# Performance work log

Hardware: AMD Instinct MI355X
Metric: run time of the kernel (lower is better)

Reference implementation:

```python
import math
import jax, jax.numpy as jnp
import numpy as np

SR = 48000
FRAME_HOP = 240
F0_MIN = 20.0
F0_MAX = 5000.0
F0_BINS = 64
VEL_DIM = 8
N_HARM = 128
NOISE_FFT = 1024
N_NOISE = NOISE_FFT // 2 + 1
HOP = NOISE_FFT // 4
PAD = NOISE_FFT // 2


def lin_interp(x, size):
    # matches F.interpolate(mode='linear', align_corners=False) along last axis
    T_in = x.shape[-1]
    pos = (jnp.arange(size, dtype=jnp.float32) + 0.5) * (T_in / size) - 0.5
    pos = jnp.clip(pos, 0.0, T_in - 1.0)
    lo = jnp.floor(pos).astype(jnp.int32)
    hi = jnp.minimum(lo + 1, T_in - 1)
    fr = pos - lo.astype(jnp.float32)
    return x[..., lo] * (1.0 - fr) + x[..., hi] * fr


def encode_f0(f0):
    f0s = jnp.clip(f0, F0_MIN, None)
    fn = jnp.clip((jnp.log(f0s) - math.log(F0_MIN)) / (math.log(F0_MAX) - math.log(F0_MIN)), 0.0, 1.0)
    i = jnp.arange(1, F0_BINS // 2 + 1, dtype=jnp.float32)
    ang = math.pi * i * fn[..., None]  # (B,T,bins/2)
    enc = jnp.stack([jnp.sin(ang), jnp.cos(ang)], axis=-1).reshape(f0.shape + (F0_BINS,))
    return enc * (f0 > 0).astype(jnp.float32)[..., None]


def encode_velocity(vel):
    vn = jnp.clip(vel.astype(jnp.float32) / 7.0, 0.0, 1.0)
    i = jnp.arange(1, VEL_DIM // 2 + 1, dtype=jnp.float32)
    ang = math.pi * i * vn[..., None]
    return jnp.stack([jnp.sin(ang), jnp.cos(ang)], axis=-1).reshape(vel.shape + (VEL_DIM,))


def gru(x, W_ih, W_hh, b_ih, b_hh):
    # torch nn.GRU, 1 layer, batch_first; gate order r,z,n
    B, T, _ = x.shape
    H = W_hh.shape[1]
    gi = x @ W_ih.T + b_ih  # (B,T,3H)

    def step(h, g):
        gh = h @ W_hh.T + b_hh
        ir, iz, in_ = jnp.split(g, 3, axis=-1)
        hr, hz, hn = jnp.split(gh, 3, axis=-1)
        r = jax.nn.sigmoid(ir + hr)
        z = jax.nn.sigmoid(iz + hz)
        n = jnp.tanh(in_ + r * hn)
        h = (1.0 - z) * n + z * h
        return h, h

    _, hs = jax.lax.scan(step, jnp.zeros((B, H), x.dtype), jnp.swapaxes(gi, 0, 1))
    return jnp.swapaxes(hs, 0, 1)


def harmonic_synth(harm_amps, f0_hz, n_samples, inh):
    # harm_amps (B,T,N), f0_hz (B,T), inh (B,) -> (B,S)
    B, T, N = harm_amps.shape
    a = lin_interp(jnp.transpose(harm_amps, (0, 2, 1)), n_samples)        # (B,N,S)
    f0_up = lin_interp(f0_hz[:, None, :], n_samples)[:, 0]               # (B,S)
    k = jnp.arange(1, N + 1, dtype=jnp.float32)
    stretch = jnp.sqrt(1.0 + inh[:, None] * k ** 2)                      # (B,N)
    inst_freq = f0_up[:, None, :] * (k[None, :] * stretch)[:, :, None]   # (B,N,S)
    mask = (inst_freq < SR * 0.45).astype(a.dtype)
    f0_mean = f0_up.mean(axis=-1)
    n_active = jnp.maximum((k[None, :] * f0_mean[:, None] < SR * 0.45).sum(axis=1), 1).astype(a.dtype)
    phase = jnp.cumsum(2.0 * jnp.pi * inst_freq / SR, axis=-1)
    sig = (a * mask * jnp.sin(phase)).sum(axis=1)
    return sig / n_active[:, None]


def noise_synth(noise_mags, f0_hz, n_samples, noise):
    # noise_mags (B,T,513), noise (B,S) -> (B,S)
    B, T, N = noise_mags.shape
    window = 0.5 - 0.5 * jnp.cos(2.0 * jnp.pi * jnp.arange(NOISE_FFT, dtype=jnp.float32) / NOISE_FFT)  # hann, periodic
    padded = jnp.pad(noise, ((0, 0), (PAD, PAD)), mode='reflect')
    T_stft = 1 + n_samples // HOP
    idx = jnp.arange(T_stft)[:, None] * HOP + jnp.arange(NOISE_FFT)[None, :]  # (T_stft, n_fft)
    frames = padded[:, idx] * window                                          # (B,T_stft,n_fft)
    spec = jnp.fft.rfft(frames)                                               # (B,T_stft,513)
    mag_up = lin_interp(jnp.transpose(noise_mags, (0, 2, 1)), T_stft)         # (B,513,T_stft)
    f0_mean = jnp.clip(f0_hz, F0_MIN, None).mean(axis=1)                      # (B,)
    freqs = jnp.arange(N_NOISE, dtype=jnp.float32) * (SR / NOISE_FFT)
    src = jnp.clip(freqs[None, :] / f0_mean[:, None] * (N / N_HARM), 0.0, N - 1.0)  # (B,513)
    lo = src.astype(jnp.int32)
    hi = jnp.minimum(lo + 1, N - 1)
    fr = (src - lo.astype(jnp.float32))[:, :, None]
    lo_e = jnp.broadcast_to(lo[:, :, None], (B, N_NOISE, T_stft))
    hi_e = jnp.broadcast_to(hi[:, :, None], (B, N_NOISE, T_stft))
    v_lo = jnp.take_along_axis(mag_up, lo_e, axis=1)
    v_hi = jnp.take_along_axis(mag_up, hi_e, axis=1)
    mag_abs = v_lo + fr * (v_hi - v_lo)                                       # (B,513,T_stft)
    shaped = spec * jnp.transpose(mag_abs, (0, 2, 1))                         # (B,T_stft,513)
    tframes = jnp.fft.irfft(shaped, n=NOISE_FFT) * window                     # (B,T_stft,n_fft)
    Lp = NOISE_FFT + (T_stft - 1) * HOP
    flat = idx.reshape(-1)
    ola = jnp.zeros((B, Lp), jnp.float32).at[:, flat].add(tframes.reshape(B, -1))
    wsq = jnp.zeros((Lp,), jnp.float32).at[flat].add(jnp.tile(window ** 2, T_stft))
    out = ola / jnp.where(wsq > 1e-11, wsq, 1.0)
    return out[:, PAD:PAD + n_samples]


def ddsp_forward(f0_hz, loudness_db, noise_L, noise_R,
                 W_pre1, b_pre1, W_pre2, b_pre2, W_ih, W_hh, b_ih, b_hh,
                 W_post, b_post, W_harm, b_harm, W_amp, b_amp,
                 W_noise, b_noise, W_namp, b_namp, W_B, b_B, velocity):
    B, T = f0_hz.shape
    n_samples = T * FRAME_HOP
    feat = jnp.concatenate([encode_f0(f0_hz),
                            jnp.broadcast_to(encode_velocity(velocity)[:, None, :], (B, T, VEL_DIM))], axis=-1)
    feat = jax.nn.relu(feat @ W_pre1 + b_pre1)
    feat = jax.nn.relu(feat @ W_pre2 + b_pre2)
    feat = gru(feat, W_ih, W_hh, b_ih, b_hh)
    feat = jax.nn.relu(feat @ W_post + b_post)
    # stereo heads stacked on channel axis c in {L,R}
    harm_dist = jax.nn.softmax(jnp.einsum('btd,cdn->cbtn', feat, W_harm) + b_harm[:, None, None, :], axis=-1)
    harm_amp = jax.nn.softplus(jnp.einsum('btd,cd->cbt', feat, W_amp) + b_amp[:, None, None])
    harm_amps = harm_dist * harm_amp[..., None]                               # (2,B,T,128)
    nmag = jax.nn.sigmoid(jnp.einsum('btd,cdn->cbtn', feat, W_noise) + b_noise[:, None, None, :])
    nmag = nmag * jax.nn.softplus(jnp.einsum('btd,cd->cbt', feat, W_namp) + b_namp[:, None, None])[..., None]
    f0_mean = jnp.clip(f0_hz, F0_MIN, None).mean(axis=1)
    midi = 69.0 + 12.0 * jnp.log2(f0_mean / 440.0)
    b_max = 0.0008 * jnp.exp(-(midi - 21.0) / 88.0 * math.log(10.0))
    inh = jax.nn.sigmoid(feat @ W_B + b_B[0]).mean(axis=1) * b_max           # inh_scale = 1.0
    hL = harmonic_synth(harm_amps[0], f0_hz, n_samples, inh)
    hR = harmonic_synth(harm_amps[1], f0_hz, n_samples, inh)
    nL = noise_synth(nmag[0], f0_hz, n_samples, noise_L)
    nR = noise_synth(nmag[1], f0_hz, n_samples, noise_R)
    lo_up = lin_interp((10.0 ** (loudness_db / 20.0))[:, None, :], n_samples)[:, 0]
    return jnp.stack([(hL + nL) * lo_up, (hR + nR) * lo_up], axis=1)         # (B,2,S)


def setup_inputs() -> dict:
    key = jax.random.key(0)
    ks = iter(jax.random.split(key, 40))
    B, T = 2, 400
    S = T * FRAME_HOP
    rnd = lambda shape, s=0.05: jax.random.normal(next(ks), shape, jnp.float32) * s
    d = {}
    d['f0_hz'] = 100.0 + 400.0 * jax.random.uniform(next(ks), (B, T), jnp.float32)
    d['loudness_db'] = -30.0 + 5.0 * jax.random.normal(next(ks), (B, T), jnp.float32)
    d['noise_L'] = jax.random.normal(next(ks), (B, S), jnp.float32)
    d['noise_R'] = jax.random.normal(next(ks), (B, S), jnp.float32)
    d['W_pre1'] = rnd((72, 128)); d['b_pre1'] = rnd((128,))
    d['W_pre2'] = rnd((128, 128)); d['b_pre2'] = rnd((128,))
    d['W_ih'] = rnd((192, 128)); d['W_hh'] = rnd((192, 64))
    d['b_ih'] = rnd((192,)); d['b_hh'] = rnd((192,))
    d['W_post'] = rnd((64, 128)); d['b_post'] = rnd((128,))
    d['W_harm'] = rnd((2, 128, N_HARM)); d['b_harm'] = rnd((2, N_HARM))
    d['W_amp'] = rnd((2, 128)); d['b_amp'] = rnd((2,))
    d['W_noise'] = rnd((2, 128, N_NOISE)); d['b_noise'] = rnd((2, N_NOISE)) - 3.0
    d['W_namp'] = rnd((2, 128)); d['b_namp'] = rnd((2,)) - 3.0
    d['W_B'] = rnd((128,)); d['b_B'] = rnd((1,)) - 5.0
    d['velocity'] = jax.random.randint(next(ks), (B,), 0, 8, dtype=jnp.int32)
    return d


def reference(f0_hz, loudness_db, noise_L, noise_R,
              W_pre1, b_pre1, W_pre2, b_pre2, W_ih, W_hh, b_ih, b_hh,
              W_post, b_post, W_harm, b_harm, W_amp, b_amp,
              W_noise, b_noise, W_namp, b_namp, W_B, b_B, velocity):
    return ddsp_forward(f0_hz, loudness_db, noise_L, noise_R,
                        W_pre1, b_pre1, W_pre2, b_pre2, W_ih, W_hh, b_ih, b_hh,
                        W_post, b_post, W_harm, b_harm, W_amp, b_amp,
                        W_noise, b_noise, W_namp, b_namp, W_B, b_B, velocity)
```

## Files before the change

### kernel.cpp

```cpp
#include <hip/hip_runtime.h>
#include <math.h>

#define Tn   400
#define Bn   2
#define Sn   96000
#define NHh  128
#define NNn  513
#define NFFT 1024
#define HOPs 256
#define PADs 512
#define TS   376
#define LPn  97024
#define CUT  21600.0f
#define DPI  3.14159265358979323846

__device__ __forceinline__ float sigmoidf_(float x){ return 1.0f/(1.0f+expf(-x)); }
__device__ __forceinline__ float softplusf_(float x){ return fmaxf(x,0.0f)+log1pf(expf(-fabsf(x))); }
__device__ __forceinline__ float fsigmoid_(float x){ return __fdividef(1.0f, 1.0f + __expf(-x)); }
__device__ __forceinline__ float ftanh_(float x){
  float e = __expf(fminf(fmaxf(2.0f*x, -30.0f), 30.0f));
  return __fdividef(e - 1.0f, e + 1.0f);
}

__global__ void __launch_bounds__(128) k_frame1(
    const float* f0, const int* vel,
    const float* Wp1, const float* bp1,
    const float* Wp2, const float* bp2,
    const float* Wih, const float* bih,
    float* gi) {
  int bt = blockIdx.x; int b = bt / Tn, t = bt % Tn;
  __shared__ float x[72];
  __shared__ float y1[128];
  __shared__ float y2[128];
  int tid = threadIdx.x;
  if (tid < 72) {
    if (tid < 64) {
      float fv = f0[b*Tn+t];
      float fsv = fmaxf(fv, 20.0f);
      float fn = (logf(fsv) - 2.99573227355399f) * (1.0f/5.52146091786225f);
      fn = fminf(fmaxf(fn,0.0f),1.0f);
      int j = (tid>>1) + 1;
      float ang = (float)DPI * (float)j * fn;
      x[tid] = (tid & 1) ? cosf(ang) : sinf(ang);
    } else {
      int i = tid - 64;
      float vn = fminf(fmaxf((float)vel[b]*(1.0f/7.0f),0.0f),1.0f);
      int j = (i>>1)+1;
      float ang = (float)DPI * (float)j * vn;
      x[tid] = (i & 1) ? cosf(ang) : sinf(ang);
    }
  }
  __syncthreads();
  {
    float a = bp1[tid];
    #pragma unroll 8
    for (int i=0;i<72;i++) a += x[i]*Wp1[i*128+tid];
    y1[tid] = fmaxf(a,0.0f);
  }
  __syncthreads();
  {
    float a = bp2[tid];
    #pragma unroll 8
    for (int i=0;i<128;i++) a += y1[i]*Wp2[i*128+tid];
    y2[tid] = fmaxf(a,0.0f);
  }
  __syncthreads();
  float* gout = gi + ((size_t)b*Tn + t)*192;
  for (int g = tid; g < 192; g += 128) {
    float s = bih[g];
    const float* wr = Wih + g*128;
    #pragma unroll 8
    for (int d=0; d<128; d++) s += y2[d]*wr[d];
    gout[g] = s;
  }
}

#define RL(x, l) __int_as_float(__builtin_amdgcn_readlane(__float_as_int(x), (l)))

#define MVP(B) { \
  a0 = RL(h,(B)+0)*w0.x;            a1 = RL(h,(B)+1)*w0.y;            a2 = RL(h,(B)+2)*w0.z;            a3 = RL(h,(B)+3)*w0.w; \
  a0 = fmaf(RL(h,(B)+4),  w1.x,a0); a1 = fmaf(RL(h,(B)+5),  w1.y,a1); a2 = fmaf(RL(h,(B)+6),  w1.z,a2); a3 = fmaf(RL(h,(B)+7),  w1.w,a3); \
  a0 = fmaf(RL(h,(B)+8),  w2.x,a0); a1 = fmaf(RL(h,(B)+9),  w2.y,a1); a2 = fmaf(RL(h,(B)+10), w2.z,a2); a3 = fmaf(RL(h,(B)+11), w2.w,a3); \
  a0 = fmaf(RL(h,(B)+12), w3.x,a0); a1 = fmaf(RL(h,(B)+13), w3.y,a1); a2 = fmaf(RL(h,(B)+14), w3.z,a2); a3 = fmaf(RL(h,(B)+15), w3.w,a3); \
  a0 = fmaf(RL(h,(B)+16), w4.x,a0); a1 = fmaf(RL(h,(B)+17), w4.y,a1); a2 = fmaf(RL(h,(B)+18), w4.z,a2); a3 = fmaf(RL(h,(B)+19), w4.w,a3); \
  a0 = fmaf(RL(h,(B)+20), w5.x,a0); a1 = fmaf(RL(h,(B)+21), w5.y,a1); a2 = fmaf(RL(h,(B)+22), w5.z,a2); a3 = fmaf(RL(h,(B)+23), w5.w,a3); \
  a0 = fmaf(RL(h,(B)+24), w6.x,a0); a1 = fmaf(RL(h,(B)+25), w6.y,a1); a2 = fmaf(RL(h,(B)+26), w6.z,a2); a3 = fmaf(RL(h,(B)+27), w6.w,a3); \
  a0 = fmaf(RL(h,(B)+28), w7.x,a0); a1 = fmaf(RL(h,(B)+29), w7.y,a1); a2 = fmaf(RL(h,(B)+30), w7.z,a2); a3 = fmaf(RL(h,(B)+31), w7.w,a3); }

__global__ void __launch_bounds__(384, 1) k_grufft(
    const float* __restrict__ gi, const float* __restrict__ Whh,
    const float* __restrict__ bhh, float* __restrict__ hsout,
    const float* __restrict__ noiseL, const float* __restrict__ noiseR,
    float2* __restrict__ spec) {
  __shared__ float sp[768];
  __shared__ float re[1024], im[1024];
  __shared__ float twc[512], tws[512];
  __shared__ float wdw[1024];
  int j = threadIdx.x;

  if (blockIdx.x >= 2) {
    if (j >= 256) return;
    int idx = blockIdx.x - 2;
    int sig = idx / TS, t = idx % TS;
    int b = sig >> 1, c = sig & 1;
    const float* noise = (c==0 ? noiseL : noiseR) + (size_t)b*Sn;
    int tid = j;
    for (int q=tid; q<512; q+=256) {
      float ang = (float)(2.0*DPI) * (float)q * (1.0f/1024.0f);
      twc[q] = cosf(ang); tws[q] = sinf(ang);
    }
    for (int i=tid; i<1024; i+=256)
      wdw[i] = 0.5f - 0.5f*cosf((float)(2.0*DPI)*(float)i*(1.0f/1024.0f));
    __syncthreads();
    for (int i=tid;i<1024;i+=256) {
      int q = t*HOPs + i - PADs;
      if (q < 0) q = -q;
      if (q >= Sn) q = 2*Sn - 2 - q;
      float v = noise[q]*wdw[i];
      int br = (int)(__brev((unsigned)i) >> 22);
      re[br] = v; im[br] = 0.0f;
    }
    __syncthreads();
    for (int st=1; st<=10; st++) {
      int half = 1<<(st-1);
      #pragma unroll
      for (int w=0;w<2;w++) {
        int bid = tid + w*256;
        int pos = bid & (half-1);
        int i0 = ((bid >> (st-1)) << st) + pos;
        int i1 = i0 + half;
        int q = pos << (10-st);
        float cr = twc[q], ci = -tws[q];
        float xr = re[i1], xi = im[i1];
        float tr = cr*xr - ci*xi, ti = cr*xi + ci*xr;
        float ar = re[i0], ai = im[i0];
        re[i1] = ar - tr; im[i1] = ai - ti;
        re[i0] = ar + tr; im[i0] = ai + ti;
      }
      __syncthreads();
    }
    float2* so = spec + ((size_t)sig*TS + t)*NNn;
    for (int k=tid;k<=512;k+=256) so[k] = make_float2(re[k], im[k]);
    return;
  }

  int b = blockIdx.x;
  const float* gib = gi + (size_t)b*Tn*192;
  float* hb_ = hsout + (size_t)b*Tn*64;
  int wv = j >> 6, lane = j & 63;
  int p = wv & 1;
  int row = (wv >> 1)*64 + lane;
  const float4* W4 = (const float4*)(Whh + (size_t)row*64 + p*32);
  float4 w0=W4[0], w1=W4[1], w2=W4[2], w3=W4[3];
  float4 w4=W4[4], w5=W4[5], w6=W4[6], w7=W4[7];
  float br = bhh[lane], bz = bhh[64+lane], bn = bhh[128+lane];
  float h = 0.0f;
  float ga[8], gz[8], gn[8], hist[8];
  #pragma unroll
  for (int i=0;i<8;i++) {
    ga[i] = gib[(size_t)i*192 + lane];
    gz[i] = gib[(size_t)i*192 + 64 + lane];
    gn[i] = gib[(size_t)i*192 + 128 + lane];
  }
  int par = 0;
  for (int c=0;c<50;c++) {
    #pragma unroll
    for (int i=0;i<8;i++) {
      float a0,a1,a2,a3;
      if (p == 0) { MVP(0) } else { MVP(32) }
      sp[par*384 + row*2 + p] = (a0+a1)+(a2+a3);
      __syncthreads();
      const float2* spp = (const float2*)(sp + par*384);
      float2 vr = spp[lane];
      float2 vz = spp[64+lane];
      float2 vn = spp[128+lane];
      float rg_ = fsigmoid_(ga[i] + br + vr.x + vr.y);
      float zg  = fsigmoid_(gz[i] + bz + vz.x + vz.y);
      float ng  = ftanh_(gn[i] + rg_*(bn + vn.x + vn.y));
      h = (1.0f - zg)*ng + zg*h;
      hist[i] = h;
      par ^= 1;
    }
    if (wv == 0) {
      int t0 = c*8;
      #pragma unroll
      for (int i=0;i<8;i++) hb_[(size_t)(t0+i)*64 + lane] = hist[i];
    }
    if (c < 49) {
      int t1 = (c+1)*8;
      #pragma unroll
      for (int i=0;i<8;i++) {
        ga[i] = gib[(size_t)(t1+i)*192 + lane];
        gz[i] = gib[(size_t)(t1+i)*192 + 64 + lane];
        gn[i] = gib[(size_t)(t1+i)*192 + 128 + lane];
      }
    }
  }
}

__global__ void __launch_bounds__(256) k_heads(
    const float* hs, const float* Wpost, const float* bpost,
    const float* Wharm, const float* bharm,
    const float* Wamp, const float* bamp,
    const float* Wnoise, const float* bnoise,
    const float* Wnamp, const float* bnamp,
    const float* WB, const float* bB,
    float* harm, float* nmag, float* fs) {
  int bt = blockIdx.x; int b = bt / Tn, t = bt % Tn;
  __shared__ float h64[64];
  __shared__ float fp[128];
  __shared__ float lg[256];
  __shared__ float red[8];
  int tid = threadIdx.x;
  if (tid < 64) h64[tid] = hs[((size_t)b*Tn+t)*64+tid];
  __syncthreads();
  if (tid < 128) {
    float a = bpost[tid];
    #pragma unroll 8
    for (int i=0;i<64;i++) a += h64[i]*Wpost[i*128+tid];
    fp[tid] = fmaxf(a,0.0f);
  }
  __syncthreads();
  {
    int c = tid >> 7, n = tid & 127;
    float a = bharm[c*128+n];
    const float* w = Wharm + (size_t)c*128*128 + n;
    #pragma unroll 8
    for (int d=0;d<128;d++) a += fp[d]*w[d*128];
    lg[tid] = a;
  }
  __syncthreads();
  if (tid < 2) {
    const float* l = lg + tid*128;
    float mx = l[0];
    for (int n=1;n<128;n++) mx = fmaxf(mx,l[n]);
    float sm = 0.f; for (int n=0;n<128;n++) sm += expf(l[n]-mx);
    red[tid] = mx; red[2+tid] = sm;
    float aa = bamp[tid];
    for (int d=0;d<128;d++) aa += fp[d]*Wamp[tid*128+d];
    red[4+tid] = softplusf_(aa);
    float na = bnamp[tid];
    for (int d=0;d<128;d++) na += fp[d]*Wnamp[tid*128+d];
    red[6+tid] = softplusf_(na);
  } else if (tid == 2) {
    float bb = bB[0];
    for (int d=0;d<128;d++) bb += fp[d]*WB[d];
    atomicAdd(&fs[6+b], sigmoidf_(bb));
  }
  __syncthreads();
  {
    int c = tid >> 7, n = tid & 127;
    float v = expf(lg[tid]-red[c]) / red[2+c] * red[4+c];
    harm[(((size_t)c*Bn + b)*Tn + t)*128 + n] = v;
  }
  for (int o = tid; o < 2*NNn; o += 256) {
    int c = (o < NNn) ? 0 : 1; int n = o - c*NNn;
    float a = bnoise[c*NNn+n];
    const float* w = Wnoise + (size_t)c*128*NNn + n;
    #pragma unroll 8
    for (int d=0;d<128;d++) a += fp[d]*w[(size_t)d*NNn];
    nmag[(((size_t)c*Bn + b)*Tn + t)*NNn + n] = sigmoidf_(a) * red[6+c];
  }
}

__global__ void k_setupinh(const float* f0, float* fs, double* P, double* rk) {
  int tid = threadIdx.x;
  __shared__ double inh_s[2];
  if (tid < 2) {
    int b = tid;
    const float* f = f0 + b*Tn;
    double sm = 0.0;
    for (int t=0;t<Tn;t++) sm += fmax((double)f[t], 20.0);
    float f0m = (float)(sm / (double)Tn);
    fs[b] = f0m;
    float midi = 69.0f + 12.0f * log2f(f0m/440.0f);
    float bmax = 0.0008f * expf(-(midi-21.0f)*(1.0f/88.0f) * 2.302585093f);
    fs[2+b] = bmax;
    double* Pb = P + b*Tn;
    double acc = 0.0;
    for (int m=0;m<Tn;m++){ Pb[m] = acc; if (m < Tn-1) acc += (double)f[m] + (double)f[m+1]; }
    double Ctot = 120.0*((double)f[0] + Pb[Tn-1] + (double)f[Tn-1]);
    double fupmean = Ctot / (double)Sn;
    int cnt = 0;
    for (int k=1;k<=NHh;k++) if ((float)k * (float)fupmean < CUT) cnt++;
    if (cnt < 1) cnt = 1;
    fs[4+b] = (float)cnt;
    float inh = fs[6+b]*(1.0f/(float)Tn) * bmax;
    fs[8+b] = inh;
    inh_s[b] = (double)inh;
  }
  __syncthreads();
  int b = tid >> 7, k = (tid & 127) + 1;
  double kk = (double)k;
  rk[b*128 + (k-1)] = kk * sqrt(1.0 + inh_s[b]*kk*kk);
}

__global__ void __launch_bounds__(256) k_harmnoise(
    const float* __restrict__ f0, const float* __restrict__ harm,
    const double* __restrict__ P, const double* __restrict__ rk,
    const float* __restrict__ fs, float* __restrict__ sigh,
    const float2* __restrict__ spec, const float* __restrict__ nmag,
    float* __restrict__ ola) {
  __shared__ double rks[128];
  __shared__ float  rkf[128];
  __shared__ float re[1024], im[1024];
  __shared__ float twc[512], tws[512];
  __shared__ float wdw[1024];
  int tid = threadIdx.x;

  if (blockIdx.x < 750) {
    int b = blockIdx.x / 375;
    int s = (blockIdx.x % 375)*256 + tid;
    if (tid < 128) {
      double r = rk[b*128+tid];
      rks[tid] = r; rkf[tid] = (float)r;
    }
    __syncthreads();
    const float* f = f0 + b*Tn;
    float posf = ((float)s + 0.5f) * (400.0f/96000.0f) - 0.5f;
    posf = fminf(fmaxf(posf, 0.0f), 399.0f);
    int lo = (int)floorf(posf);
    int hi = min(lo+1, 399);
    float fr = posf - (float)lo;
    float f0up = f[lo]*(1.0f-fr) + f[hi]*fr;
    double C;
    if (s < 120) {
      C = (double)(s+1) * (double)f[0];
    } else if (s < 95880) {
      int m = (s-120)/240;
      int q = s - 120 - 240*m;
      double fm = (double)f[m], fm1 = (double)f[m+1];
      double jp = (double)(q+1);
      C = 120.0*((double)f[0] + P[b*Tn+m]) + jp*fm + (fm1-fm)*jp*jp*(1.0/480.0);
    } else {
      C = 120.0*((double)f[0] + P[b*Tn+399]) + (double)(s-95880+1)*(double)f[399];
    }
    double Phi = C * (2.0*DPI/48000.0);
    const float* hLlo = harm + (((size_t)0*Bn + b)*Tn + lo)*128;
    const float* hLhi = harm + (((size_t)0*Bn + b)*Tn + hi)*128;
    const float* hRlo = harm + (((size_t)1*Bn + b)*Tn + lo)*128;
    const float* hRhi = harm + (((size_t)1*Bn + b)*Tn + hi)*128;
    float accL=0.f, accR=0.f;
    for (int k=0;k<128;k++) {
      float finst = f0up * rkf[k];
      if (finst < CUT) {
        double u = rks[k]*Phi * (1.0/(2.0*DPI));
        u -= floor(u);
        float sv = __sinf((float)u * 6.28318530717959f);
        float aL = hLlo[k]*(1.0f-fr) + hLhi[k]*fr;
        float aR = hRlo[k]*(1.0f-fr) + hRhi[k]*fr;
        accL += aL*sv; accR += aR*sv;
      }
    }
    float na = fs[4+b];
    sigh[((size_t)b*2+0)*Sn + s] = accL/na;
    sigh[((size_t)b*2+1)*Sn + s] = accR/na;
    return;
  }

  int idx = blockIdx.x - 750;
  int sig = idx / TS, t = idx % TS;
  int b = sig >> 1, c = sig & 1;
  for (int q=tid; q<512; q+=256) {
    float ang = (float)(2.0*DPI) * (float)q * (1.0f/1024.0f);
    twc[q] = cosf(ang); tws[q] = sinf(ang);
  }
  for (int i=tid; i<1024; i+=256)
    wdw[i] = 0.5f - 0.5f*cosf((float)(2.0*DPI)*(float)i*(1.0f/1024.0f));
  float f0m = fs[b];
  float pp = ((float)t + 0.5f) * (400.0f/376.0f) - 0.5f;
  pp = fminf(fmaxf(pp,0.0f),399.0f);
  int tlo = (int)floorf(pp); int thi = min(tlo+1, 399); float tfr = pp - (float)tlo;
  const float* nm = nmag + (((size_t)c*Bn + b)*Tn)*NNn;
  const float2* so = spec + ((size_t)sig*TS + t)*NNn;
  for (int k=tid;k<=512;k+=256) {
    float src = (float)k * 46.875f / f0m * (513.0f/128.0f);
    src = fminf(fmaxf(src,0.0f),512.0f);
    int flo = (int)src; int fhi = min(flo+1,512); float ffr = src - (float)flo;
    float vlo = nm[(size_t)tlo*NNn+flo]*(1.0f-tfr) + nm[(size_t)thi*NNn+flo]*tfr;
    float vhi = nm[(size_t)tlo*NNn+fhi]*(1.0f-tfr) + nm[(size_t)thi*NNn+fhi]*tfr;
    float mag = vlo + ffr*(vhi-vlo);
    float2 v = so[k];
    re[k] = v.x*mag; im[k] = v.y*mag;
  }
  __syncthreads();
  for (int k=tid+513; k<1024; k+=256) {
    re[k] = re[1024-k]; im[k] = -im[1024-k];
  }
  __syncthreads();
  for (int i=tid;i<1024;i+=256) {
    int jx = (int)(__brev((unsigned)i)>>22);
    if (i < jx) {
      float a=re[i]; re[i]=re[jx]; re[jx]=a;
      float bb=im[i]; im[i]=im[jx]; im[jx]=bb;
    }
  }
  __syncthreads();
  for (int st=1; st<=10; st++) {
    int half = 1<<(st-1);
    #pragma unroll
    for (int w=0;w<2;w++) {
      int bid = tid + w*256;
      int pos = bid & (half-1);
      int i0 = ((bid >> (st-1)) << st) + pos;
      int i1 = i0 + half;
      int q = pos << (10-st);
      float cr = twc[q], ci = tws[q];
      float xr = re[i1], xi = im[i1];
      float tr = cr*xr - ci*xi, ti = cr*xi + ci*xr;
      float ar = re[i0], ai = im[i0];
      re[i1] = ar - tr; im[i1] = ai - ti;
      re[i0] = ar + tr; im[i0] = ai + ti;
    }
    __syncthreads();
  }
  float* olab = ola + (size_t)sig*LPn;
  for (int i=tid;i<1024;i+=256) {
    float y = re[i] * (1.0f/1024.0f) * wdw[i];
    atomicAdd(&olab[t*HOPs + i], y);
  }
}

__global__ void __launch_bounds__(256) k_final(
    const float* loud, const float* sigh, const float* ola, float* out) {
  int b = blockIdx.y;
  int s = blockIdx.x*256 + threadIdx.x;
  float posf = ((float)s + 0.5f)*(400.0f/96000.0f) - 0.5f;
  posf = fminf(fmaxf(posf,0.0f),399.0f);
  int lo=(int)floorf(posf); int hi=min(lo+1,399); float fr=posf-(float)lo;
  const float* ld = loud + b*Tn;
  float lv = exp10f(ld[lo]*0.05f)*(1.0f-fr) + exp10f(ld[hi]*0.05f)*fr;
  int p = PADs + s;
  float wsq;
  if (s >= 511 && s <= 95743) {
    wsq = 1.5f;
  } else {
    int t0 = (p >= 1023) ? ((p - 1023 + 255) >> 8) : 0;
    int t1 = min(TS-1, p >> 8);
    wsq = 0.0f;
    for (int t=t0;t<=t1;t++) {
      int i = p - (t<<8);
      float w = 0.5f - 0.5f*cosf((float)(2.0*DPI)*(float)i*(1.0f/1024.0f));
      wsq += w*w;
    }
  }
  float denom = (wsq > 1e-11f) ? wsq : 1.0f;
  for (int c=0;c<2;c++) {
    float hv = sigh[((size_t)b*2+c)*Sn+s];
    float nv = ola[(size_t)(b*2+c)*LPn + p] / denom;
    out[((size_t)b*2+c)*Sn + s] = (hv + nv)*lv;
  }
}

extern "C" void kernel_launch(void* const* d_in, const int* in_sizes, int n_in,
                              void* d_out, int out_size, void* d_ws, size_t ws_size,
                              hipStream_t stream) {
  const float* f0    = (const float*)d_in[0];
  const float* loud  = (const float*)d_in[1];
  const float* nL    = (const float*)d_in[2];
  const float* nR    = (const float*)d_in[3];
  const float* Wp1   = (const float*)d_in[4];  const float* bp1 = (const float*)d_in[5];
  const float* Wp2   = (const float*)d_in[6];  const float* bp2 = (const float*)d_in[7];
  const float* Wih   = (const float*)d_in[8];  const float* Whh = (const float*)d_in[9];
  const float* bih   = (const float*)d_in[10]; const float* bhh = (const float*)d_in[11];
  const float* Wpost = (const float*)d_in[12]; const float* bpost=(const float*)d_in[13];
  const float* Wharm = (const float*)d_in[14]; const float* bharm=(const float*)d_in[15];
  const float* Wamp  = (const float*)d_in[16]; const float* bamp =(const float*)d_in[17];
  const float* Wnoise= (const float*)d_in[18]; const float* bnoise=(const float*)d_in[19];
  const float* Wnamp = (const float*)d_in[20]; const float* bnamp=(const float*)d_in[21];
  const float* WB    = (const float*)d_in[22]; const float* bB  = (const float*)d_in[23];
  const int*   vel   = (const int*)d_in[24];
  float* out = (float*)d_out;

  char* w = (char*)d_ws;
  double* P    = (double*)w; w += (size_t)Bn*Tn*sizeof(double);
  double* rk   = (double*)w; w += (size_t)Bn*128*sizeof(double);
  float* gi    = (float*)w;  w += (size_t)Bn*Tn*192*sizeof(float);
  float* hsb   = (float*)w;  w += (size_t)Bn*Tn*64*sizeof(float);
  float* harm  = (float*)w;  w += (size_t)2*Bn*Tn*128*sizeof(float);
  float* nmag  = (float*)w;  w += (size_t)2*Bn*Tn*NNn*sizeof(float);
  float* sigh  = (float*)w;  w += (size_t)Bn*2*Sn*sizeof(float);
  float* ola   = (float*)w;  w += (size_t)Bn*2*LPn*sizeof(float);
  float* fscal = (float*)w;  w += 32*sizeof(float);
  float2* spec = (float2*)w; w += (size_t)4*TS*NNn*sizeof(float2);

  hipMemsetAsync(ola, 0, (size_t)Bn*2*LPn*sizeof(float) + 32*sizeof(float), stream);

  k_frame1<<<Bn*Tn, 128, 0, stream>>>(f0, vel, Wp1,bp1, Wp2,bp2, Wih,bih, gi);
  k_grufft<<<2 + 4*TS, 384, 0, stream>>>(gi, Whh, bhh, hsb, nL, nR, spec);
  k_heads<<<Bn*Tn, 256, 0, stream>>>(hsb, Wpost,bpost, Wharm,bharm, Wamp,bamp,
                                     Wnoise,bnoise, Wnamp,bnamp, WB,bB,
                                     harm, nmag, fscal);
  k_setupinh<<<1, 256, 0, stream>>>(f0, fscal, P, rk);
  k_harmnoise<<<750 + 4*TS, 256, 0, stream>>>(f0, harm, P, rk, fscal, sigh,
                                              spec, nmag, ola);
  dim3 gf(Sn/256, Bn);
  k_final<<<gf, 256, 0, stream>>>(loud, sigh, ola, out);
}
```

Before: 461.2 us.

## Fold memset and inharmonicity setup into frame kernel; restructure GRU recurrence

The output-buffer memset and the single-block setup kernel are folded into extra blocks of the first frame kernel. The per-harmonic stretch factors are now computed inline in the harmonic synthesis kernel, which removes two launches. The GRU recurrence changes from a readlane-based matvec over 6 waves to 12 matvec waves that read h from shared memory, plus one wave that applies the gate nonlinearities. That adds a second barrier per time step. The fused GRU/FFT kernel now launches 832 threads per block, so the FFT blocks also carry many idle threads, which may reduce their occupancy.

```diff
diff --git a/kernel.cpp b/kernel.cpp
--- a/kernel.cpp
+++ b/kernel.cpp
@@ -22,17 +22,50 @@
   return __fdividef(e - 1.0f, e + 1.0f);
 }
 
-__global__ void __launch_bounds__(128) k_frame1(
+__global__ void __launch_bounds__(128) k_frame1z(
     const float* f0, const int* vel,
     const float* Wp1, const float* bp1,
     const float* Wp2, const float* bp2,
     const float* Wih, const float* bih,
-    float* gi) {
-  int bt = blockIdx.x; int b = bt / Tn, t = bt % Tn;
+    float* gi, float4* olaz, float* fs, double* P) {
+  int blk = blockIdx.x;
+  int tid = threadIdx.x;
+  if (blk >= Bn*Tn) {
+    if (blk == Bn*Tn) {
+      int b = tid;
+      if (b < Bn) {
+        const float* f = f0 + b*Tn;
+        double sm = 0.0;
+        for (int t=0;t<Tn;t++) sm += fmax((double)f[t], 20.0);
+        float f0m = (float)(sm / (double)Tn);
+        fs[b] = f0m;
+        float midi = 69.0f + 12.0f * log2f(f0m/440.0f);
+        fs[2+b] = 0.0008f * expf(-(midi-21.0f)*(1.0f/88.0f) * 2.302585093f);
+        double* Pb = P + b*Tn;
+        double acc = 0.0;
+        for (int m=0;m<Tn;m++){ Pb[m] = acc; if (m < Tn-1) acc += (double)f[m] + (double)f[m+1]; }
+        double Ctot = 120.0*((double)f[0] + Pb[Tn-1] + (double)f[Tn-1]);
+        double fupmean = Ctot / (double)Sn;
+        int cnt = 0;
+        for (int k=1;k<=NHh;k++) if ((float)k * (float)fupmean < CUT) cnt++;
+        if (cnt < 1) cnt = 1;
+        fs[4+b] = (float)cnt;
+        fs[6+b] = 0.0f;
+      }
+    } else {
+      int base = (blk - (Bn*Tn+1))*512 + tid;
+      #pragma unroll
+      for (int r=0;r<4;r++) {
+        int idx = base + r*128;
+        if (idx < 97024) olaz[idx] = make_float4(0.f,0.f,0.f,0.f);
+      }
+    }
+    return;
+  }
+  int b = blk / Tn, t = blk % Tn;
   __shared__ float x[72];
   __shared__ float y1[128];
   __shared__ float y2[128];
-  int tid = threadIdx.x;
   if (tid < 72) {
     if (tid < 64) {
       float fv = f0[b*Tn+t];
@@ -75,23 +108,12 @@
   }
 }
 
-#define RL(x, l) __int_as_float(__builtin_amdgcn_readlane(__float_as_int(x), (l)))
-
-#define MVP(B) { \
-  a0 = RL(h,(B)+0)*w0.x;            a1 = RL(h,(B)+1)*w0.y;            a2 = RL(h,(B)+2)*w0.z;            a3 = RL(h,(B)+3)*w0.w; \
-  a0 = fmaf(RL(h,(B)+4),  w1.x,a0); a1 = fmaf(RL(h,(B)+5),  w1.y,a1); a2 = fmaf(RL(h,(B)+6),  w1.z,a2); a3 = fmaf(RL(h,(B)+7),  w1.w,a3); \
-  a0 = fmaf(RL(h,(B)+8),  w2.x,a0); a1 = fmaf(RL(h,(B)+9),  w2.y,a1); a2 = fmaf(RL(h,(B)+10), w2.z,a2); a3 = fmaf(RL(h,(B)+11), w2.w,a3); \
-  a0 = fmaf(RL(h,(B)+12), w3.x,a0); a1 = fmaf(RL(h,(B)+13), w3.y,a1); a2 = fmaf(RL(h,(B)+14), w3.z,a2); a3 = fmaf(RL(h,(B)+15), w3.w,a3); \
-  a0 = fmaf(RL(h,(B)+16), w4.x,a0); a1 = fmaf(RL(h,(B)+17), w4.y,a1); a2 = fmaf(RL(h,(B)+18), w4.z,a2); a3 = fmaf(RL(h,(B)+19), w4.w,a3); \
-  a0 = fmaf(RL(h,(B)+20), w5.x,a0); a1 = fmaf(RL(h,(B)+21), w5.y,a1); a2 = fmaf(RL(h,(B)+22), w5.z,a2); a3 = fmaf(RL(h,(B)+23), w5.w,a3); \
-  a0 = fmaf(RL(h,(B)+24), w6.x,a0); a1 = fmaf(RL(h,(B)+25), w6.y,a1); a2 = fmaf(RL(h,(B)+26), w6.z,a2); a3 = fmaf(RL(h,(B)+27), w6.w,a3); \
-  a0 = fmaf(RL(h,(B)+28), w7.x,a0); a1 = fmaf(RL(h,(B)+29), w7.y,a1); a2 = fmaf(RL(h,(B)+30), w7.z,a2); a3 = fmaf(RL(h,(B)+31), w7.w,a3); }
-
-__global__ void __launch_bounds__(384, 1) k_grufft(
+__global__ void __launch_bounds__(832, 1) k_grufft(
     const float* __restrict__ gi, const float* __restrict__ Whh,
     const float* __restrict__ bhh, float* __restrict__ hsout,
     const float* __restrict__ noiseL, const float* __restrict__ noiseR,
     float2* __restrict__ spec) {
+  __shared__ float h[64];
   __shared__ float sp[768];
   __shared__ float re[1024], im[1024];
   __shared__ float twc[512], tws[512];
@@ -148,51 +170,70 @@
   const float* gib = gi + (size_t)b*Tn*192;
   float* hb_ = hsout + (size_t)b*Tn*64;
   int wv = j >> 6, lane = j & 63;
-  int p = wv & 1;
-  int row = (wv >> 1)*64 + lane;
-  const float4* W4 = (const float4*)(Whh + (size_t)row*64 + p*32);
-  float4 w0=W4[0], w1=W4[1], w2=W4[2], w3=W4[3];
-  float4 w4=W4[4], w5=W4[5], w6=W4[6], w7=W4[7];
-  float br = bhh[lane], bz = bhh[64+lane], bn = bhh[128+lane];
-  float h = 0.0f;
-  float ga[8], gz[8], gn[8], hist[8];
-  #pragma unroll
-  for (int i=0;i<8;i++) {
-    ga[i] = gib[(size_t)i*192 + lane];
-    gz[i] = gib[(size_t)i*192 + 64 + lane];
-    gn[i] = gib[(size_t)i*192 + 128 + lane];
-  }
-  int par = 0;
+  int p = wv / 3;
+  int row = (wv % 3)*64 + lane;
+  float4 w0,w1,w2,w3;
+  if (j < 768) {
+    const float4* W4 = (const float4*)(Whh + (size_t)row*64 + p*16);
+    w0=W4[0]; w1=W4[1]; w2=W4[2]; w3=W4[3];
+    if (j < 64) h[j] = 0.0f;
+  }
+  int u = lane;
+  float hu = 0.0f, br=0.f, bz=0.f, bn=0.f;
+  float ga[8], gz_[8], gn_[8], hist[8];
+  if (j >= 768) {
+    br = bhh[u]; bz = bhh[64+u]; bn = bhh[128+u];
+    #pragma unroll
+    for (int i=0;i<8;i++) {
+      ga[i]  = gib[(size_t)i*192 + u];
+      gz_[i] = gib[(size_t)i*192 + 64 + u];
+      gn_[i] = gib[(size_t)i*192 + 128 + u];
+    }
+  }
+  __syncthreads();
+
   for (int c=0;c<50;c++) {
     #pragma unroll
     for (int i=0;i<8;i++) {
-      float a0,a1,a2,a3;
-      if (p == 0) { MVP(0) } else { MVP(32) }
-      sp[par*384 + row*2 + p] = (a0+a1)+(a2+a3);
+      if (j < 768) {
+        const float4* h4 = (const float4*)h;
+        float4 x0=h4[p*4+0], x1=h4[p*4+1], x2=h4[p*4+2], x3=h4[p*4+3];
+        float a0,a1,a2,a3;
+        a0 = w0.x*x0.x; a1 = w0.y*x0.y; a2 = w0.z*x0.z; a3 = w0.w*x0.w;
+        a0 = fmaf(w1.x,x1.x,a0); a1 = fmaf(w1.y,x1.y,a1);
+        a2 = fmaf(w1.z,x1.z,a2); a3 = fmaf(w1.w,x1.w,a3);
+        a0 = fmaf(w2.x,x2.x,a0); a1 = fmaf(w2.y,x2.y,a1);
+        a2 = fmaf(w2.z,x2.z,a2); a3 = fmaf(w2.w,x2.w,a3);
+        a0 = fmaf(w3.x,x3.x,a0); a1 = fmaf(w3.y,x3.y,a1);
+        a2 = fmaf(w3.z,x3.z,a2); a3 = fmaf(w3.w,x3.w,a3);
+        sp[p*192 + row] = (a0+a1)+(a2+a3);
+      }
       __syncthreads();
-      const float2* spp = (const float2*)(sp + par*384);
-      float2 vr = spp[lane];
-      float2 vz = spp[64+lane];
-      float2 vn = spp[128+lane];
-      float rg_ = fsigmoid_(ga[i] + br + vr.x + vr.y);
-      float zg  = fsigmoid_(gz[i] + bz + vz.x + vz.y);
-      float ng  = ftanh_(gn[i] + rg_*(bn + vn.x + vn.y));
-      h = (1.0f - zg)*ng + zg*h;
-      hist[i] = h;
-      par ^= 1;
-    }
-    if (wv == 0) {
+      if (j >= 768) {
+        float mr = (sp[u]      + sp[192+u])     + (sp[384+u]     + sp[576+u]);
+        float mz = (sp[64+u]   + sp[192+64+u])  + (sp[384+64+u]  + sp[576+64+u]);
+        float mn = (sp[128+u]  + sp[192+128+u]) + (sp[384+128+u] + sp[576+128+u]);
+        float rg = fsigmoid_(ga[i]  + br + mr);
+        float zg = fsigmoid_(gz_[i] + bz + mz);
+        float ng = ftanh_(gn_[i] + rg*(bn + mn));
+        hu = (1.0f - zg)*ng + zg*hu;
+        h[u] = hu;
+        hist[i] = hu;
+      }
+      __syncthreads();
+    }
+    if (j >= 768) {
       int t0 = c*8;
       #pragma unroll
-      for (int i=0;i<8;i++) hb_[(size_t)(t0+i)*64 + lane] = hist[i];
-    }
-    if (c < 49) {
-      int t1 = (c+1)*8;
-      #pragma unroll
-      for (int i=0;i<8;i++) {
-        ga[i] = gib[(size_t)(t1+i)*192 + lane];
-        gz[i] = gib[(size_t)(t1+i)*192 + 64 + lane];
-        gn[i] = gib[(size_t)(t1+i)*192 + 128 + lane];
+      for (int i=0;i<8;i++) hb_[(size_t)(t0+i)*64 + u] = hist[i];
+      if (c < 49) {
+        int t1 = t0 + 8;
+        #pragma unroll
+        for (int i=0;i<8;i++) {
+          ga[i]  = gib[(size_t)(t1+i)*192 + u];
+          gz_[i] = gib[(size_t)(t1+i)*192 + 64 + u];
+          gn_[i] = gib[(size_t)(t1+i)*192 + 128 + u];
+        }
       }
     }
   }
@@ -263,42 +304,10 @@
   }
 }
 
-__global__ void k_setupinh(const float* f0, float* fs, double* P, double* rk) {
-  int tid = threadIdx.x;
-  __shared__ double inh_s[2];
-  if (tid < 2) {
-    int b = tid;
-    const float* f = f0 + b*Tn;
-    double sm = 0.0;
-    for (int t=0;t<Tn;t++) sm += fmax((double)f[t], 20.0);
-    float f0m = (float)(sm / (double)Tn);
-    fs[b] = f0m;
-    float midi = 69.0f + 12.0f * log2f(f0m/440.0f);
-    float bmax = 0.0008f * expf(-(midi-21.0f)*(1.0f/88.0f) * 2.302585093f);
-    fs[2+b] = bmax;
-    double* Pb = P + b*Tn;
-    double acc = 0.0;
-    for (int m=0;m<Tn;m++){ Pb[m] = acc; if (m < Tn-1) acc += (double)f[m] + (double)f[m+1]; }
-    double Ctot = 120.0*((double)f[0] + Pb[Tn-1] + (double)f[Tn-1]);
-    double fupmean = Ctot / (double)Sn;
-    int cnt = 0;
-    for (int k=1;k<=NHh;k++) if ((float)k * (float)fupmean < CUT) cnt++;
-    if (cnt < 1) cnt = 1;
-    fs[4+b] = (float)cnt;
-    float inh = fs[6+b]*(1.0f/(float)Tn) * bmax;
-    fs[8+b] = inh;
-    inh_s[b] = (double)inh;
-  }
-  __syncthreads();
-  int b = tid >> 7, k = (tid & 127) + 1;
-  double kk = (double)k;
-  rk[b*128 + (k-1)] = kk * sqrt(1.0 + inh_s[b]*kk*kk);
-}
-
 __global__ void __launch_bounds__(256) k_harmnoise(
     const float* __restrict__ f0, const float* __restrict__ harm,
-    const double* __restrict__ P, const double* __restrict__ rk,
-    const float* __restrict__ fs, float* __restrict__ sigh,
+    const double* __restrict__ P, const float* __restrict__ fs,
+    float* __restrict__ sigh,
     const float2* __restrict__ spec, const float* __restrict__ nmag,
     float* __restrict__ ola) {
   __shared__ double rks[128];
@@ -312,7 +321,10 @@
     int b = blockIdx.x / 375;
     int s = (blockIdx.x % 375)*256 + tid;
     if (tid < 128) {
-      double r = rk[b*128+tid];
+      float inhf = fs[6+b]*(1.0f/(float)Tn) * fs[2+b];
+      double inh = (double)inhf;
+      double kk = (double)(tid+1);
+      double r = kk * sqrt(1.0 + inh*kk*kk);
       rks[tid] = r; rkf[tid] = (float)r;
     }
     __syncthreads();
@@ -483,16 +495,16 @@
   float* ola   = (float*)w;  w += (size_t)Bn*2*LPn*sizeof(float);
   float* fscal = (float*)w;  w += 32*sizeof(float);
   float2* spec = (float2*)w; w += (size_t)4*TS*NNn*sizeof(float2);
-
-  hipMemsetAsync(ola, 0, (size_t)Bn*2*LPn*sizeof(float) + 32*sizeof(float), stream);
-
-  k_frame1<<<Bn*Tn, 128, 0, stream>>>(f0, vel, Wp1,bp1, Wp2,bp2, Wih,bih, gi);
-  k_grufft<<<2 + 4*TS, 384, 0, stream>>>(gi, Whh, bhh, hsb, nL, nR, spec);
+  (void)rk;
+
+  int nzblk = (97024 + 511) / 512;
+  k_frame1z<<<Bn*Tn + 1 + nzblk, 128, 0, stream>>>(
+      f0, vel, Wp1,bp1, Wp2,bp2, Wih,bih, gi, (float4*)ola, fscal, P);
+  k_grufft<<<2 + 4*TS, 832, 0, stream>>>(gi, Whh, bhh, hsb, nL, nR, spec);
   k_heads<<<Bn*Tn, 256, 0, stream>>>(hsb, Wpost,bpost, Wharm,bharm, Wamp,bamp,
                                      Wnoise,bnoise, Wnamp,bnamp, WB,bB,
                                      harm, nmag, fscal);
-  k_setupinh<<<1, 256, 0, stream>>>(f0, fscal, P, rk);
-  k_harmnoise<<<750 + 4*TS, 256, 0, stream>>>(f0, harm, P, rk, fscal, sigh,
+  k_harmnoise<<<750 + 4*TS, 256, 0, stream>>>(f0, harm, P, fscal, sigh,
                                               spec, nmag, ola);
   dim3 gf(Sn/256, Bn);
   k_final<<<gf, 256, 0, stream>>>(loud, sigh, ola, out);
```

Result: faster. 391.5 us (-15.1%).
